# Kernel tuning notes

Hardware: AMD Instinct MI355X
Metric: run time of the kernel (lower is better)

Reference implementation:

```python
import jax, jax.numpy as jnp
import numpy as np

B, K = 16, 64          # batch, n_particles
IN = 128               # sensory input dim
H0, H1 = 192, 64       # wiring layer sizes (H0+H1 = state_size 256)
UNF = 6                # ode_unfolds
EPS = 1e-8
BK = B * K


def _layer_params(key, n_in, h, sigma_init=0.1):
    ks = jax.random.split(key, 11)
    u = lambda k, sh, lo, hi: jax.random.uniform(k, sh, dtype=jnp.float32) * (hi - lo) + lo
    return dict(
        gleak=u(ks[0], (h,), 0.001, 1.0),
        vleak=u(ks[1], (h,), -0.2, 0.2),
        cm=u(ks[2], (h,), 0.4, 0.6),
        iw=u(ks[3], (n_in, h), 0.001, 1.0),
        isig=u(ks[4], (n_in, h), 3.0, 8.0),
        imu=u(ks[5], (n_in, h), 0.3, 0.8),
        ierev=jax.random.normal(ks[6], (n_in, h), dtype=jnp.float32),
        w=u(ks[7], (h, h), 0.001, 1.0),
        sig=u(ks[8], (h, h), 3.0, 8.0),
        mu=u(ks[9], (h, h), 0.3, 0.8),
        erev=jax.random.normal(ks[10], (h, h), dtype=jnp.float32),
        gdiff=jnp.full((h,), sigma_init, dtype=jnp.float32),
    )


def setup_inputs() -> dict:
    key = jax.random.key(0)
    k = jax.random.split(key, 6)
    inp = {
        'x': jax.random.normal(k[0], (B, IN), dtype=jnp.float32),
        'particles': jax.random.normal(k[1], (B, K, H0 + H1), dtype=jnp.float32) * 0.1,
        'log_weights': jnp.full((B, K), -np.log(K), dtype=jnp.float32),
        'noise0': jax.random.normal(k[2], (UNF, BK, H0), dtype=jnp.float32),
        'noise1': jax.random.normal(k[3], (UNF, BK, H1), dtype=jnp.float32),
    }
    p0 = _layer_params(k[4], IN, H0)
    p1 = _layer_params(k[5], H0, H1)
    for n, v in p0.items():
        inp[n + '0'] = v
    for n, v in p1.items():
        inp[n + '1'] = v
    return inp


def _drift(v, x, gleak, vleak, cm, iw, isig, imu, ierev, w, sig, mu, erev):
    # x: [BK, n_in], v: [BK, h]
    ia = jax.nn.relu(iw) * jax.nn.sigmoid(isig * (x[:, :, None] - imu))   # [BK, n_in, h]
    w_num_in = jnp.einsum('bih,ih->bh', ia, ierev)
    w_den_in = ia.sum(axis=1)
    wa = jax.nn.relu(w) * jax.nn.sigmoid(sig * (v[:, :, None] - mu))      # [BK, h, h]
    w_num = jnp.einsum('bih,ih->bh', wa, erev) + w_num_in
    w_den = wa.sum(axis=1) + w_den_in
    gl = jax.nn.relu(gleak)
    c = jax.nn.relu(cm) + EPS
    return (gl * vleak + w_num - (gl + w_den) * v) / c


def _unfold(v0, x, noise, gdiff, dt, drift_params):
    sdt = jnp.sqrt(dt)
    def step(v, n):
        d = _drift(v, x, *drift_params)
        return v + d * dt + gdiff * sdt * n, None
    v, _ = jax.lax.scan(step, v0, noise)
    return v


def reference(x, particles, log_weights, noise0, noise1,
              gleak0, vleak0, cm0, iw0, isig0, imu0, ierev0, w0, sig0, mu0, erev0, gdiff0,
              gleak1, vleak1, cm1, iw1, isig1, imu1, ierev1, w1, sig1, mu1, erev1, gdiff1):
    dt = jnp.float32(1.0 / UNF)  # elapsed=1.0 split over n_unfolds
    xk = jnp.broadcast_to(x[:, None, :], (B, K, IN)).reshape(BK, IN)
    v0 = particles[..., :H0].reshape(BK, H0)
    v1 = particles[..., H0:].reshape(BK, H1)
    p0 = (gleak0, vleak0, cm0, iw0, isig0, imu0, ierev0, w0, sig0, mu0, erev0)
    p1 = (gleak1, vleak1, cm1, iw1, isig1, imu1, ierev1, w1, sig1, mu1, erev1)
    s0 = _unfold(v0, xk, noise0, gdiff0, dt, p0)      # layer 0 output feeds layer 1
    s1 = _unfold(v1, s0, noise1, gdiff1, dt, p1)
    new_particles = jnp.concatenate([s0.reshape(B, K, H0), s1.reshape(B, K, H1)], axis=-1)
    # uniform weights -> ESS = K, resampler is a no-op; output = weighted particle mean
    wts = jax.nn.softmax(log_weights, axis=1)[..., None]   # [B, K, 1]
    output = (wts * s1.reshape(B, K, H1)).sum(axis=1)      # [B, H1]
    return output, new_particles, log_weights
```

## Files before the change

### kernel.cpp

```cpp
#include <hip/hip_runtime.h>
#include <math.h>

constexpr int B   = 16;
constexpr int K   = 64;
constexpr int BK  = B * K;
constexpr int IN  = 128;
constexpr int H0  = 192;
constexpr int H1  = 64;
constexpr int UNF = 6;
constexpr float EPS = 1e-8f;
constexpr float DT  = 1.0f / 6.0f;
constexpr float L2E = 1.4426950408889634f;

static __device__ __forceinline__ float rcpf(float x) {
    return __builtin_amdgcn_rcpf(x);
}
static __device__ __forceinline__ float exp2_fast(float x) {
#if __has_builtin(__builtin_amdgcn_exp2f)
    return __builtin_amdgcn_exp2f(x);
#else
    return exp2f(x);
#endif
}
static __device__ __forceinline__ float sig_from_t(float t) {
    return rcpf(1.0f + exp2_fast(t));
}

constexpr int NPACK    = H0 * H0 + H0 * H1 + H1 * H1;
constexpr int NPACKBLK = NPACK / 256;
__global__ __launch_bounds__(256) void prep_kernel(
    const float* __restrict__ w0,  const float* __restrict__ sig0,
    const float* __restrict__ mu0, const float* __restrict__ erev0,
    const float* __restrict__ iw1, const float* __restrict__ isig1,
    const float* __restrict__ imu1,const float* __restrict__ ierev1,
    const float* __restrict__ w1,  const float* __restrict__ sig1,
    const float* __restrict__ mu1, const float* __restrict__ erev1,
    const float* __restrict__ x,   const float* __restrict__ iw0,
    const float* __restrict__ isig0,const float* __restrict__ imu0,
    const float* __restrict__ ierev0,
    float4* __restrict__ pack0, float4* __restrict__ packi1,
    float4* __restrict__ pack1,
    float* __restrict__ in_num, float* __restrict__ in_den)
{
    __shared__ float xs[IN];
    if (blockIdx.x < NPACKBLK) {
        const int t = blockIdx.x * 256 + threadIdx.x;
        constexpr int N0 = H0 * H0;
        constexpr int N1 = H0 * H1;
        if (t < N0) {
            const float wv = fmaxf(w0[t], 0.0f);
            pack0[t] = make_float4(wv, sig0[t] * L2E, sig0[t] * mu0[t] * L2E,
                                   wv * erev0[t]);
        } else if (t < N0 + N1) {
            const int u = t - N0;
            const float wv = fmaxf(iw1[u], 0.0f);
            packi1[u] = make_float4(wv, isig1[u] * L2E,
                                    isig1[u] * imu1[u] * L2E, wv * ierev1[u]);
        } else {
            const int u = t - N0 - N1;
            const float wv = fmaxf(w1[u], 0.0f);
            pack1[u] = make_float4(wv, sig1[u] * L2E, sig1[u] * mu1[u] * L2E,
                                   wv * erev1[u]);
        }
    } else {
        const int b = blockIdx.x - NPACKBLK;
        const int h = threadIdx.x;
        if (h < IN) xs[h] = x[b * IN + h];
        __syncthreads();
        if (h < H0) {
            float num = 0.0f, den = 0.0f;
            #pragma unroll 4
            for (int i = 0; i < IN; ++i) {
                const int idx = i * H0 + h;
                const float wv = fmaxf(iw0[idx], 0.0f);
                const float t  = isig0[idx] * L2E * (imu0[idx] - xs[i]);
                const float a  = wv * sig_from_t(t);
                num = fmaf(a, ierev0[idx], num);
                den += a;
            }
            in_num[b * H0 + h] = num;
            in_den[b * H0 + h] = den;
        }
    }
}

template <int LEN>
static __device__ __forceinline__ void sweep0_body(
    const float4* __restrict__ pp,
    const float* vsbase, int ibase,
    float num[4], float den[4])
{
    #pragma unroll 8
    for (int ii = 0; ii < LEN; ++ii) {
        const float4 p  = pp[(size_t)ii * H0];
        const float4 vv = *(const float4*)(vsbase + (ibase + ii) * 4);
        float s;
        s = sig_from_t(fmaf(-p.y, vv.x, p.z));
        num[0] = fmaf(s, p.w, num[0]); den[0] = fmaf(s, p.x, den[0]);
        s = sig_from_t(fmaf(-p.y, vv.y, p.z));
        num[1] = fmaf(s, p.w, num[1]); den[1] = fmaf(s, p.x, den[1]);
        s = sig_from_t(fmaf(-p.y, vv.z, p.z));
        num[2] = fmaf(s, p.w, num[2]); den[2] = fmaf(s, p.x, den[2]);
        s = sig_from_t(fmaf(-p.y, vv.w, p.z));
        num[3] = fmaf(s, p.w, num[3]); den[3] = fmaf(s, p.x, den[3]);
    }
}

__global__ __launch_bounds__(960) void fused_unfold_kernel(
    const float* __restrict__ particles,
    const float* __restrict__ noise0,
    const float* __restrict__ noise1,
    const float* __restrict__ log_weights,
    const float* __restrict__ gleak0, const float* __restrict__ vleak0,
    const float* __restrict__ cm0,    const float* __restrict__ gdiff0,
    const float* __restrict__ gleak1, const float* __restrict__ vleak1,
    const float* __restrict__ cm1,    const float* __restrict__ gdiff1,
    const float4* __restrict__ pack0,
    const float4* __restrict__ packi1,
    const float4* __restrict__ pack1,
    const float* __restrict__ in_num,
    const float* __restrict__ in_den,
    float* __restrict__ outp,
    float* __restrict__ out_y,
    float* __restrict__ out_lw)
{
    const int tid = threadIdx.x;
    const int h   = tid % H0;
    const int q   = tid / H0;
    const int bk0 = blockIdx.x * 4;
    const int b   = blockIdx.x >> 4;
    const int k0  = (blockIdx.x & 15) * 4;

    const int h1  = tid & 63;
    const int qq  = tid >> 6;

    __shared__ __align__(16) float vs[H0][4];
    __shared__ float2 part0[5][4][H0];
    __shared__ __align__(16) float v1s[H1][4];
    __shared__ float2 part1[8][4][H1];
    __shared__ float  w4[4];

    if (tid < 64) {
        const float lw = log_weights[b * K + tid];
        out_lw[b * K + tid] = lw;
        float mx = lw;
        #pragma unroll
        for (int o = 32; o > 0; o >>= 1) mx = fmaxf(mx, __shfl_xor(mx, o));
        const float e = __expf(lw - mx);
        float ssum = e;
        #pragma unroll
        for (int o = 32; o > 0; o >>= 1) ssum += __shfl_xor(ssum, o);
        if (tid >= k0 && tid < k0 + 4) w4[tid - k0] = e / ssum;
    }

    float nz1[UNF];
    if (tid < 256) {
        v1s[h1][qq] = particles[(bk0 + qq) * 256 + H0 + h1];
        #pragma unroll
        for (int s = 0; s < UNF; ++s)
            nz1[s] = noise1[s * (BK * H1) + (bk0 + qq) * H1 + h1];
    }

    float nz[UNF];
    if (q < 4) {
        vs[h][q] = particles[(bk0 + q) * 256 + h];
        #pragma unroll
        for (int s = 0; s < UNF; ++s)
            nz[s] = noise0[s * (BK * H0) + (bk0 + q) * H0 + h];
    }

    const float gl    = fmaxf(gleak0[h], 0.0f);
    const float glvl  = gl * vleak0[h];
    const float cinv  = rcpf(fmaxf(cm0[h], 0.0f) + EPS);
    const float gd    = gdiff0[h] * sqrtf(DT);
    const float innum = in_num[b * H0 + h];
    const float inden = in_den[b * H0 + h];
    __syncthreads();

    const int ibase = (q == 4) ? 160 : 40 * q;
    const float4* pp = pack0 + (size_t)ibase * H0 + h;
    for (int step = 0; step < UNF; ++step) {
        float num[4] = {0.f, 0.f, 0.f, 0.f};
        float den[4] = {0.f, 0.f, 0.f, 0.f};
        if (q == 4) sweep0_body<32>(pp, &vs[0][0], ibase, num, den);
        else        sweep0_body<40>(pp, &vs[0][0], ibase, num, den);
        #pragma unroll
        for (int m = 0; m < 4; ++m)
            part0[q][m][h] = make_float2(num[m], den[m]);
        __syncthreads();
        if (q < 4) {
            float tn = innum, td = inden;
            #pragma unroll
            for (int j = 0; j < 5; ++j) {
                const float2 t = part0[j][q][h];
                tn += t.x; td += t.y;
            }
            const float vh = vs[h][q];
            const float d  = (glvl + tn - (gl + td) * vh) * cinv;
            vs[h][q] = fmaf(gd, nz[step], fmaf(d, DT, vh));
        }
        __syncthreads();
    }

    if (q < 4) outp[(bk0 + q) * 256 + h] = vs[h][q];

    float gl1 = 0.f, glvl1 = 0.f, cinv1 = 0.f, gd1 = 0.f;
    float in1n[4] = {0.f, 0.f, 0.f, 0.f};
    float in1d[4] = {0.f, 0.f, 0.f, 0.f};
    if (tid < 512) {
        gl1   = fmaxf(gleak1[h1], 0.0f);
        glvl1 = gl1 * vleak1[h1];
        cinv1 = rcpf(fmaxf(cm1[h1], 0.0f) + EPS);
        gd1   = gdiff1[h1] * sqrtf(DT);
        #pragma unroll 4
        for (int ii = 0; ii < 24; ++ii) {
            const int i = qq * 24 + ii;
            const float4 p  = packi1[i * H1 + h1];
            const float4 vv = *(const float4*)&vs[i][0];
            float s;
            s = sig_from_t(fmaf(-p.y, vv.x, p.z));
            in1n[0] = fmaf(s, p.w, in1n[0]); in1d[0] = fmaf(s, p.x, in1d[0]);
            s = sig_from_t(fmaf(-p.y, vv.y, p.z));
            in1n[1] = fmaf(s, p.w, in1n[1]); in1d[1] = fmaf(s, p.x, in1d[1]);
            s = sig_from_t(fmaf(-p.y, vv.z, p.z));
            in1n[2] = fmaf(s, p.w, in1n[2]); in1d[2] = fmaf(s, p.x, in1d[2]);
            s = sig_from_t(fmaf(-p.y, vv.w, p.z));
            in1n[3] = fmaf(s, p.w, in1n[3]); in1d[3] = fmaf(s, p.x, in1d[3]);
        }
    }
    __syncthreads();

    for (int step = 0; step < UNF; ++step) {
        if (tid < 512) {
            float num[4], den[4];
            #pragma unroll
            for (int m = 0; m < 4; ++m) { num[m] = in1n[m]; den[m] = in1d[m]; }
            #pragma unroll
            for (int ii = 0; ii < 8; ++ii) {
                const int i = qq * 8 + ii;
                const float4 p  = pack1[i * H1 + h1];
                const float4 vv = *(const float4*)&v1s[i][0];
                float s;
                s = sig_from_t(fmaf(-p.y, vv.x, p.z));
                num[0] = fmaf(s, p.w, num[0]); den[0] = fmaf(s, p.x, den[0]);
                s = sig_from_t(fmaf(-p.y, vv.y, p.z));
                num[1] = fmaf(s, p.w, num[1]); den[1] = fmaf(s, p.x, den[1]);
                s = sig_from_t(fmaf(-p.y, vv.z, p.z));
                num[2] = fmaf(s, p.w, num[2]); den[2] = fmaf(s, p.x, den[2]);
                s = sig_from_t(fmaf(-p.y, vv.w, p.z));
                num[3] = fmaf(s, p.w, num[3]); den[3] = fmaf(s, p.x, den[3]);
            }
            #pragma unroll
            for (int m = 0; m < 4; ++m)
                part1[qq][m][h1] = make_float2(num[m], den[m]);
        }
        __syncthreads();
        if (tid < 256) {
            float tn = 0.f, td = 0.f;
            #pragma unroll
            for (int j = 0; j < 8; ++j) {
                const float2 t = part1[j][qq][h1];
                tn += t.x; td += t.y;
            }
            const float vh = v1s[h1][qq];
            const float d  = (glvl1 + tn - (gl1 + td) * vh) * cinv1;
            v1s[h1][qq] = fmaf(gd1, nz1[step], fmaf(d, DT, vh));
        }
        __syncthreads();
    }

    if (tid < 256)
        outp[(bk0 + qq) * 256 + H0 + h1] = v1s[h1][qq];

    if (tid < 64) {
        const float acc = w4[0] * v1s[tid][0] + w4[1] * v1s[tid][1]
                        + w4[2] * v1s[tid][2] + w4[3] * v1s[tid][3];
        atomicAdd(&out_y[b * H1 + tid], acc);
    }
}

extern "C" void kernel_launch(void* const* d_in, const int* in_sizes, int n_in,
                              void* d_out, int out_size, void* d_ws, size_t ws_size,
                              hipStream_t stream) {
    const float* x           = (const float*)d_in[0];
    const float* particles   = (const float*)d_in[1];
    const float* log_weights = (const float*)d_in[2];
    const float* noise0      = (const float*)d_in[3];
    const float* noise1      = (const float*)d_in[4];
    const float* gleak0 = (const float*)d_in[5];
    const float* vleak0 = (const float*)d_in[6];
    const float* cm0    = (const float*)d_in[7];
    const float* iw0    = (const float*)d_in[8];
    const float* isig0  = (const float*)d_in[9];
    const float* imu0   = (const float*)d_in[10];
    const float* ierev0 = (const float*)d_in[11];
    const float* w0     = (const float*)d_in[12];
    const float* sig0   = (const float*)d_in[13];
    const float* mu0    = (const float*)d_in[14];
    const float* erev0  = (const float*)d_in[15];
    const float* gdiff0 = (const float*)d_in[16];
    const float* gleak1 = (const float*)d_in[17];
    const float* vleak1 = (const float*)d_in[18];
    const float* cm1    = (const float*)d_in[19];
    const float* iw1    = (const float*)d_in[20];
    const float* isig1  = (const float*)d_in[21];
    const float* imu1   = (const float*)d_in[22];
    const float* ierev1 = (const float*)d_in[23];
    const float* w1     = (const float*)d_in[24];
    const float* sig1   = (const float*)d_in[25];
    const float* mu1    = (const float*)d_in[26];
    const float* erev1  = (const float*)d_in[27];
    const float* gdiff1 = (const float*)d_in[28];

    float* out    = (float*)d_out;
    float* out_y  = out;
    float* out_np = out + B * H1;
    float* out_lw = out + B * H1 + BK * 256;

    float* ws      = (float*)d_ws;
    float4* pack0  = (float4*)(ws);
    float4* packi1 = (float4*)(ws + 4 * 36864);
    float4* pack1  = (float4*)(ws + 4 * (36864 + 12288));
    float*  in_num0 = ws + 4 * (36864 + 12288 + 4096);
    float*  in_den0 = in_num0 + B * H0;

    hipMemsetAsync(out_y, 0, B * H1 * sizeof(float), stream);

    prep_kernel<<<NPACKBLK + B, 256, 0, stream>>>(
        w0, sig0, mu0, erev0, iw1, isig1, imu1, ierev1, w1, sig1, mu1, erev1,
        x, iw0, isig0, imu0, ierev0,
        pack0, packi1, pack1, in_num0, in_den0);

    fused_unfold_kernel<<<BK / 4, 960, 0, stream>>>(
        particles, noise0, noise1, log_weights,
        gleak0, vleak0, cm0, gdiff0,
        gleak1, vleak1, cm1, gdiff1,
        pack0, packi1, pack1, in_num0, in_den0,
        out_np, out_y, out_lw);
}
```

Before: 195.2 us.

## Double-buffer layer-0 weight loads and spread layer-1 input drift over more warps

The layer-0 sweep now works in chunks of 8 rows, with the next chunk's packed float4 parameters prefetched into registers while the current chunk is computed, so global load latency is hidden behind the sigmoid math. The layer-1 input-drift precompute is spread over 768 threads (16 rows each) instead of 512 (24 rows each). The extra four warp groups leave their partial sums in additional part1 slots, which stay fixed across the unfold steps and are summed at each reduction. The cost is higher register pressure from the pa/pb/vvr buffers under a 960-thread launch bound, which could cause spills.

```diff
diff --git a/kernel.cpp b/kernel.cpp
--- a/kernel.cpp
+++ b/kernel.cpp
@@ -84,25 +84,41 @@
     }
 }
 
-template <int LEN>
-static __device__ __forceinline__ void sweep0_body(
+template <int NCHUNK>
+static __device__ __forceinline__ void sweep0_pipe(
     const float4* __restrict__ pp,
-    const float* vsbase, int ibase,
+    const float4* __restrict__ vp,
     float num[4], float den[4])
 {
-    #pragma unroll 8
-    for (int ii = 0; ii < LEN; ++ii) {
-        const float4 p  = pp[(size_t)ii * H0];
-        const float4 vv = *(const float4*)(vsbase + (ibase + ii) * 4);
-        float s;
-        s = sig_from_t(fmaf(-p.y, vv.x, p.z));
-        num[0] = fmaf(s, p.w, num[0]); den[0] = fmaf(s, p.x, den[0]);
-        s = sig_from_t(fmaf(-p.y, vv.y, p.z));
-        num[1] = fmaf(s, p.w, num[1]); den[1] = fmaf(s, p.x, den[1]);
-        s = sig_from_t(fmaf(-p.y, vv.z, p.z));
-        num[2] = fmaf(s, p.w, num[2]); den[2] = fmaf(s, p.x, den[2]);
-        s = sig_from_t(fmaf(-p.y, vv.w, p.z));
-        num[3] = fmaf(s, p.w, num[3]); den[3] = fmaf(s, p.x, den[3]);
+    float4 pa[8], pb[8];
+    #pragma unroll
+    for (int j = 0; j < 8; ++j) pa[j] = pp[(size_t)j * H0];
+    #pragma unroll
+    for (int c = 0; c < NCHUNK; ++c) {
+        const float4* cur = (c & 1) ? pb : pa;
+        float4*       nxt = (c & 1) ? pa : pb;
+        if (c + 1 < NCHUNK) {
+            #pragma unroll
+            for (int j = 0; j < 8; ++j)
+                nxt[j] = pp[(size_t)((c + 1) * 8 + j) * H0];
+        }
+        float4 vvr[8];
+        #pragma unroll
+        for (int j = 0; j < 8; ++j) vvr[j] = vp[c * 8 + j];
+        #pragma unroll
+        for (int j = 0; j < 8; ++j) {
+            const float4 p  = cur[j];
+            const float4 vv = vvr[j];
+            float s;
+            s = sig_from_t(fmaf(-p.y, vv.x, p.z));
+            num[0] = fmaf(s, p.w, num[0]); den[0] = fmaf(s, p.x, den[0]);
+            s = sig_from_t(fmaf(-p.y, vv.y, p.z));
+            num[1] = fmaf(s, p.w, num[1]); den[1] = fmaf(s, p.x, den[1]);
+            s = sig_from_t(fmaf(-p.y, vv.z, p.z));
+            num[2] = fmaf(s, p.w, num[2]); den[2] = fmaf(s, p.x, den[2]);
+            s = sig_from_t(fmaf(-p.y, vv.w, p.z));
+            num[3] = fmaf(s, p.w, num[3]); den[3] = fmaf(s, p.x, den[3]);
+        }
     }
 }
 
@@ -137,7 +153,7 @@
     __shared__ __align__(16) float vs[H0][4];
     __shared__ float2 part0[5][4][H0];
     __shared__ __align__(16) float v1s[H1][4];
-    __shared__ float2 part1[8][4][H1];
+    __shared__ float2 part1[12][4][H1];
     __shared__ float  w4[4];
 
     if (tid < 64) {
@@ -179,11 +195,12 @@
 
     const int ibase = (q == 4) ? 160 : 40 * q;
     const float4* pp = pack0 + (size_t)ibase * H0 + h;
+    const float4* vp = (const float4*)&vs[ibase][0];
     for (int step = 0; step < UNF; ++step) {
         float num[4] = {0.f, 0.f, 0.f, 0.f};
         float den[4] = {0.f, 0.f, 0.f, 0.f};
-        if (q == 4) sweep0_body<32>(pp, &vs[0][0], ibase, num, den);
-        else        sweep0_body<40>(pp, &vs[0][0], ibase, num, den);
+        if (q == 4) sweep0_pipe<4>(pp, vp, num, den);
+        else        sweep0_pipe<5>(pp, vp, num, den);
         #pragma unroll
         for (int m = 0; m < 4; ++m)
             part0[q][m][h] = make_float2(num[m], den[m]);
@@ -207,14 +224,14 @@
     float gl1 = 0.f, glvl1 = 0.f, cinv1 = 0.f, gd1 = 0.f;
     float in1n[4] = {0.f, 0.f, 0.f, 0.f};
     float in1d[4] = {0.f, 0.f, 0.f, 0.f};
-    if (tid < 512) {
+    if (tid < 768) {
         gl1   = fmaxf(gleak1[h1], 0.0f);
         glvl1 = gl1 * vleak1[h1];
         cinv1 = rcpf(fmaxf(cm1[h1], 0.0f) + EPS);
         gd1   = gdiff1[h1] * sqrtf(DT);
         #pragma unroll 4
-        for (int ii = 0; ii < 24; ++ii) {
-            const int i = qq * 24 + ii;
+        for (int ii = 0; ii < 16; ++ii) {
+            const int i = qq * 16 + ii;
             const float4 p  = packi1[i * H1 + h1];
             const float4 vv = *(const float4*)&vs[i][0];
             float s;
@@ -226,6 +243,11 @@
             in1n[2] = fmaf(s, p.w, in1n[2]); in1d[2] = fmaf(s, p.x, in1d[2]);
             s = sig_from_t(fmaf(-p.y, vv.w, p.z));
             in1n[3] = fmaf(s, p.w, in1n[3]); in1d[3] = fmaf(s, p.x, in1d[3]);
+        }
+        if (tid >= 512) {
+            #pragma unroll
+            for (int m = 0; m < 4; ++m)
+                part1[qq][m][h1] = make_float2(in1n[m], in1d[m]);
         }
     }
     __syncthreads();
@@ -258,7 +280,7 @@
         if (tid < 256) {
             float tn = 0.f, td = 0.f;
             #pragma unroll
-            for (int j = 0; j < 8; ++j) {
+            for (int j = 0; j < 12; ++j) {
                 const float2 t = part1[j][qq][h1];
                 tn += t.x; td += t.y;
             }
```

Result: slower. 250.8 us (+28.5%).

## Use 768-thread blocks, cache packed weights in registers across unfold steps

Applied to the files above, without the earlier changes.

Shrinks the fused kernel from 960 to 768 threads so layer 0 splits its 192 inputs into four even 48-row slices. Each thread now keeps the first 16 packed float4 parameter rows of its slice in registers for all six unfold steps, and layer 1 keeps its 8 pack1 rows in registers. The layer-1 input-projection sweep is spread over all 12 waves, with an extra partial reduction slot. The aim is to cut repeated global/L2 weight loads and remove the uneven fifth slice, at the cost of more register pressure and fewer threads for latency hiding.

```diff
diff --git a/kernel.cpp b/kernel.cpp
--- a/kernel.cpp
+++ b/kernel.cpp
@@ -24,6 +24,19 @@
 }
 static __device__ __forceinline__ float sig_from_t(float t) {
     return rcpf(1.0f + exp2_fast(t));
+}
+
+static __device__ __forceinline__ void rows4(const float4 p, const float4 vv,
+                                             float num[4], float den[4]) {
+    float s;
+    s = sig_from_t(fmaf(-p.y, vv.x, p.z));
+    num[0] = fmaf(s, p.w, num[0]); den[0] = fmaf(s, p.x, den[0]);
+    s = sig_from_t(fmaf(-p.y, vv.y, p.z));
+    num[1] = fmaf(s, p.w, num[1]); den[1] = fmaf(s, p.x, den[1]);
+    s = sig_from_t(fmaf(-p.y, vv.z, p.z));
+    num[2] = fmaf(s, p.w, num[2]); den[2] = fmaf(s, p.x, den[2]);
+    s = sig_from_t(fmaf(-p.y, vv.w, p.z));
+    num[3] = fmaf(s, p.w, num[3]); den[3] = fmaf(s, p.x, den[3]);
 }
 
 constexpr int NPACK    = H0 * H0 + H0 * H1 + H1 * H1;
@@ -84,29 +97,7 @@
     }
 }
 
-template <int LEN>
-static __device__ __forceinline__ void sweep0_body(
-    const float4* __restrict__ pp,
-    const float* vsbase, int ibase,
-    float num[4], float den[4])
-{
-    #pragma unroll 8
-    for (int ii = 0; ii < LEN; ++ii) {
-        const float4 p  = pp[(size_t)ii * H0];
-        const float4 vv = *(const float4*)(vsbase + (ibase + ii) * 4);
-        float s;
-        s = sig_from_t(fmaf(-p.y, vv.x, p.z));
-        num[0] = fmaf(s, p.w, num[0]); den[0] = fmaf(s, p.x, den[0]);
-        s = sig_from_t(fmaf(-p.y, vv.y, p.z));
-        num[1] = fmaf(s, p.w, num[1]); den[1] = fmaf(s, p.x, den[1]);
-        s = sig_from_t(fmaf(-p.y, vv.z, p.z));
-        num[2] = fmaf(s, p.w, num[2]); den[2] = fmaf(s, p.x, den[2]);
-        s = sig_from_t(fmaf(-p.y, vv.w, p.z));
-        num[3] = fmaf(s, p.w, num[3]); den[3] = fmaf(s, p.x, den[3]);
-    }
-}
-
-__global__ __launch_bounds__(960) void fused_unfold_kernel(
+__global__ __launch_bounds__(768) void fused_unfold_kernel(
     const float* __restrict__ particles,
     const float* __restrict__ noise0,
     const float* __restrict__ noise1,
@@ -135,9 +126,9 @@
     const int qq  = tid >> 6;
 
     __shared__ __align__(16) float vs[H0][4];
-    __shared__ float2 part0[5][4][H0];
+    __shared__ float2 part0[4][4][H0];
     __shared__ __align__(16) float v1s[H1][4];
-    __shared__ float2 part1[8][4][H1];
+    __shared__ float2 part1[12][4][H1];
     __shared__ float  w4[4];
 
     if (tid < 64) {
@@ -161,13 +152,11 @@
             nz1[s] = noise1[s * (BK * H1) + (bk0 + qq) * H1 + h1];
     }
 
+    vs[h][q] = particles[(bk0 + q) * 256 + h];
     float nz[UNF];
-    if (q < 4) {
-        vs[h][q] = particles[(bk0 + q) * 256 + h];
-        #pragma unroll
-        for (int s = 0; s < UNF; ++s)
-            nz[s] = noise0[s * (BK * H0) + (bk0 + q) * H0 + h];
-    }
+    #pragma unroll
+    for (int s = 0; s < UNF; ++s)
+        nz[s] = noise0[s * (BK * H0) + (bk0 + q) * H0 + h];
 
     const float gl    = fmaxf(gleak0[h], 0.0f);
     const float glvl  = gl * vleak0[h];
@@ -175,58 +164,67 @@
     const float gd    = gdiff0[h] * sqrtf(DT);
     const float innum = in_num[b * H0 + h];
     const float inden = in_den[b * H0 + h];
+
+    const float4* pp = pack0 + (size_t)(48 * q) * H0 + h;
+    float4 pr[16];
+    #pragma unroll
+    for (int j = 0; j < 16; ++j) pr[j] = pp[(size_t)j * H0];
+    const float4* ps = pp + (size_t)16 * H0;
+
+    const float4* vs4 = (const float4*)&vs[0][0];
     __syncthreads();
 
-    const int ibase = (q == 4) ? 160 : 40 * q;
-    const float4* pp = pack0 + (size_t)ibase * H0 + h;
     for (int step = 0; step < UNF; ++step) {
         float num[4] = {0.f, 0.f, 0.f, 0.f};
         float den[4] = {0.f, 0.f, 0.f, 0.f};
-        if (q == 4) sweep0_body<32>(pp, &vs[0][0], ibase, num, den);
-        else        sweep0_body<40>(pp, &vs[0][0], ibase, num, den);
+        #pragma unroll
+        for (int j = 0; j < 16; ++j)
+            rows4(pr[j], vs4[48 * q + j], num, den);
+        #pragma unroll 8
+        for (int ii = 0; ii < 32; ++ii)
+            rows4(ps[(size_t)ii * H0], vs4[48 * q + 16 + ii], num, den);
+
         #pragma unroll
         for (int m = 0; m < 4; ++m)
             part0[q][m][h] = make_float2(num[m], den[m]);
         __syncthreads();
-        if (q < 4) {
-            float tn = innum, td = inden;
-            #pragma unroll
-            for (int j = 0; j < 5; ++j) {
-                const float2 t = part0[j][q][h];
-                tn += t.x; td += t.y;
-            }
-            const float vh = vs[h][q];
-            const float d  = (glvl + tn - (gl + td) * vh) * cinv;
-            vs[h][q] = fmaf(gd, nz[step], fmaf(d, DT, vh));
-        }
-        __syncthreads();
-    }
-
-    if (q < 4) outp[(bk0 + q) * 256 + h] = vs[h][q];
-
-    float gl1 = 0.f, glvl1 = 0.f, cinv1 = 0.f, gd1 = 0.f;
+        float tn = innum, td = inden;
+        #pragma unroll
+        for (int j = 0; j < 4; ++j) {
+            const float2 t = part0[j][q][h];
+            tn += t.x; td += t.y;
+        }
+        const float vh = vs[h][q];
+        const float d  = (glvl + tn - (gl + td) * vh) * cinv;
+        vs[h][q] = fmaf(gd, nz[step], fmaf(d, DT, vh));
+        __syncthreads();
+    }
+
+    outp[(bk0 + q) * 256 + h] = vs[h][q];
+
+    const float gl1   = fmaxf(gleak1[h1], 0.0f);
+    const float glvl1 = gl1 * vleak1[h1];
+    const float cinv1 = rcpf(fmaxf(cm1[h1], 0.0f) + EPS);
+    const float gd1   = gdiff1[h1] * sqrtf(DT);
+
+    float4 pr1[8];
+    if (tid < 512) {
+        #pragma unroll
+        for (int j = 0; j < 8; ++j)
+            pr1[j] = pack1[(qq * 8 + j) * H1 + h1];
+    }
+
     float in1n[4] = {0.f, 0.f, 0.f, 0.f};
     float in1d[4] = {0.f, 0.f, 0.f, 0.f};
-    if (tid < 512) {
-        gl1   = fmaxf(gleak1[h1], 0.0f);
-        glvl1 = gl1 * vleak1[h1];
-        cinv1 = rcpf(fmaxf(cm1[h1], 0.0f) + EPS);
-        gd1   = gdiff1[h1] * sqrtf(DT);
-        #pragma unroll 4
-        for (int ii = 0; ii < 24; ++ii) {
-            const int i = qq * 24 + ii;
-            const float4 p  = packi1[i * H1 + h1];
-            const float4 vv = *(const float4*)&vs[i][0];
-            float s;
-            s = sig_from_t(fmaf(-p.y, vv.x, p.z));
-            in1n[0] = fmaf(s, p.w, in1n[0]); in1d[0] = fmaf(s, p.x, in1d[0]);
-            s = sig_from_t(fmaf(-p.y, vv.y, p.z));
-            in1n[1] = fmaf(s, p.w, in1n[1]); in1d[1] = fmaf(s, p.x, in1d[1]);
-            s = sig_from_t(fmaf(-p.y, vv.z, p.z));
-            in1n[2] = fmaf(s, p.w, in1n[2]); in1d[2] = fmaf(s, p.x, in1d[2]);
-            s = sig_from_t(fmaf(-p.y, vv.w, p.z));
-            in1n[3] = fmaf(s, p.w, in1n[3]); in1d[3] = fmaf(s, p.x, in1d[3]);
-        }
+    #pragma unroll 4
+    for (int ii = 0; ii < 16; ++ii) {
+        const int i = qq * 16 + ii;
+        rows4(packi1[i * H1 + h1], vs4[i], in1n, in1d);
+    }
+    if (tid >= 512) {
+        #pragma unroll
+        for (int m = 0; m < 4; ++m)
+            part1[qq][m][h1] = make_float2(in1n[m], in1d[m]);
     }
     __syncthreads();
 
@@ -236,20 +234,8 @@
             #pragma unroll
             for (int m = 0; m < 4; ++m) { num[m] = in1n[m]; den[m] = in1d[m]; }
             #pragma unroll
-            for (int ii = 0; ii < 8; ++ii) {
-                const int i = qq * 8 + ii;
-                const float4 p  = pack1[i * H1 + h1];
-                const float4 vv = *(const float4*)&v1s[i][0];
-                float s;
-                s = sig_from_t(fmaf(-p.y, vv.x, p.z));
-                num[0] = fmaf(s, p.w, num[0]); den[0] = fmaf(s, p.x, den[0]);
-                s = sig_from_t(fmaf(-p.y, vv.y, p.z));
-                num[1] = fmaf(s, p.w, num[1]); den[1] = fmaf(s, p.x, den[1]);
-                s = sig_from_t(fmaf(-p.y, vv.z, p.z));
-                num[2] = fmaf(s, p.w, num[2]); den[2] = fmaf(s, p.x, den[2]);
-                s = sig_from_t(fmaf(-p.y, vv.w, p.z));
-                num[3] = fmaf(s, p.w, num[3]); den[3] = fmaf(s, p.x, den[3]);
-            }
+            for (int ii = 0; ii < 8; ++ii)
+                rows4(pr1[ii], *(const float4*)&v1s[qq * 8 + ii][0], num, den);
             #pragma unroll
             for (int m = 0; m < 4; ++m)
                 part1[qq][m][h1] = make_float2(num[m], den[m]);
@@ -258,7 +244,7 @@
         if (tid < 256) {
             float tn = 0.f, td = 0.f;
             #pragma unroll
-            for (int j = 0; j < 8; ++j) {
+            for (int j = 0; j < 12; ++j) {
                 const float2 t = part1[j][qq][h1];
                 tn += t.x; td += t.y;
             }
@@ -331,7 +317,7 @@
         x, iw0, isig0, imu0, ierev0,
         pack0, packi1, pack1, in_num0, in_den0);
 
-    fused_unfold_kernel<<<BK / 4, 960, 0, stream>>>(
+    fused_unfold_kernel<<<BK / 4, 768, 0, stream>>>(
         particles, noise0, noise1, log_weights,
         gleak0, vleak0, cm0, gdiff0,
         gleak1, vleak1, cm1, gdiff1,
```

Measured after the change: 298.4 us. 1.53x slower.
